# Kernel tuning notes

Measured on AMD Instinct MI355X. Metric: run time of the kernel, lower is better.

Reference implementation:

```python
import jax, jax.numpy as jnp
import numpy as np

RESOLUTION = 2048
NUM_BEAMS = 256
K0 = 50.0
TWO_PI = 2.0 * np.pi


def setup_inputs() -> dict:
    key = jax.random.key(0)
    ks = jax.random.split(key, 6)
    # meshgrid buffers (indexing='ij')
    x = jnp.linspace(-1.0, 1.0, RESOLUTION, dtype=jnp.float32)
    y = jnp.linspace(-1.0, 1.0, RESOLUTION, dtype=jnp.float32)
    X, Y = jnp.meshgrid(x, y, indexing='ij')
    return {
        'theta': jax.random.uniform(ks[0], (NUM_BEAMS,), jnp.float32) * TWO_PI,
        'real': jax.random.normal(ks[1], (NUM_BEAMS,), jnp.float32) * 0.1,
        'imag': jax.random.normal(ks[2], (NUM_BEAMS,), jnp.float32) * 0.1,
        'x0': jax.random.uniform(ks[3], (NUM_BEAMS,), jnp.float32) * 2.0 - 1.0,
        'y0': jax.random.uniform(ks[4], (NUM_BEAMS,), jnp.float32) * 2.0 - 1.0,
        'log_sigma': jnp.zeros((NUM_BEAMS,), jnp.float32),
        'X': X,
        'Y': Y,
    }


def reference(theta, real, imag, x0, y0, log_sigma, X, Y):
    # Accumulate E = sum_i coeff_i * exp(i*phase_i) * envelope_i over beams,
    # carrying (E_re, E_im) through a scan so only grid-sized buffers live at once.
    def body(carry, p):
        E_re, E_im = carry
        th, re, im, px, py, ls = p
        kx = K0 * jnp.cos(th)
        ky = K0 * jnp.sin(th)
        sigma = jnp.exp(ls) + 0.001
        env = jnp.exp(-((X - px) ** 2 + (Y - py) ** 2) / sigma ** 2)
        phase = kx * X + ky * Y
        c = jnp.cos(phase)
        s = jnp.sin(phase)
        # (re + i*im) * (c + i*s) * env
        E_re = E_re + env * (re * c - im * s)
        E_im = E_im + env * (re * s + im * c)
        return (E_re, E_im), None

    params = jnp.stack([theta, real, imag, x0, y0, log_sigma], axis=1)  # [B, 6]
    zero = jnp.zeros_like(X)
    (E_re, E_im), _ = jax.lax.scan(body, (zero, zero), params)
    return E_re ** 2 + E_im ** 2  # |E|^2
```

## Files before the change

kernel.cpp:

```cpp
#include <hip/hip_runtime.h>
#include <math.h>

#define RES 2048
#define NB  256
#define PLANE (RES * NB)
#define STEP (2.0f / 2047.0f)

typedef _Float16 f16;
typedef _Float16 f16x8 __attribute__((ext_vector_type(8)));
typedef float    f32x16 __attribute__((ext_vector_type(16)));

#define AS1 __attribute__((address_space(1)))
#define AS3 __attribute__((address_space(3)))

__device__ __forceinline__ void g2l16(const void* g, void* l) {
    __builtin_amdgcn_global_load_lds((const AS1 void*)g, (AS3 void*)l, 16, 0, 0);
}

__device__ __forceinline__ f16x8 neg8(f16x8 v) {
    union { f16x8 h; unsigned int u[4]; } x;
    x.h = v;
    #pragma unroll
    for (int i = 0; i < 4; ++i) x.u[i] ^= 0x80008000u;
    return x.h;
}


__global__ __launch_bounds__(256) void tables_frag(
    const float* __restrict__ theta, const float* __restrict__ reA,
    const float* __restrict__ imA, const float* __restrict__ x0A,
    const float* __restrict__ y0A, const float* __restrict__ lsA,
    f16* __restrict__ ws)
{
    __shared__ float4 sP0[NB];
    __shared__ float4 sP1[NB];

    const int t = threadIdx.x;
    {
        const int b = t;
        const float th = theta[b];
        const float s = __sinf(th), c = __cosf(th);
        const float sig = __expf(lsA[b]) + 0.001f;
        sP0[b] = make_float4(50.0f * c, 50.0f * s, x0A[b], y0A[b]);
        sP1[b] = make_float4(reA[b], imA[b], 1.0f / (sig * sig), 0.0f);
    }
    __syncthreads();

    f16* aRe = ws;
    f16* aIm = ws + PLANE;
    f16* bRe = ws + 2 * PLANE;
    f16* bIm = ws + 3 * PLANE;

    const int gid = blockIdx.x * 256 + t;
    const int l   = gid & 63;
    const int w   = gid >> 6;
    const int grow = (w >> 4) * 32 + (l & 31);
    const int b0   = (w & 15) * 16 + (l >> 5) * 8;
    const int e    = w * 512 + (l >> 5) * 256 + (l & 31) * 8;

    const float xv = -1.0f + (float)grow * STEP;

    float aRv[8], aIv[8], bRv[8], bIv[8];
    #pragma unroll
    for (int j = 0; j < 8; ++j) {
        const int b = b0 + j;
        const float4 p0 = sP0[b];
        const float4 p1 = sP1[b];

        const float phx = p0.x * xv;
        const float snx = __sinf(phx), csx = __cosf(phx);
        const float dx = xv - p0.z;
        const float ex = __expf(-dx * dx * p1.z);
        aRv[j] = ex * (p1.x * csx - p1.y * snx);
        aIv[j] = ex * (p1.x * snx + p1.y * csx);

        const float phy = p0.y * xv;
        const float sny = __sinf(phy), csy = __cosf(phy);
        const float dy = xv - p0.w;
        const float ey = __expf(-dy * dy * p1.z);
        bRv[j] = ey * csy;
        bIv[j] = ey * sny;
    }

    union { f16 h[8]; float4 v; } p;
    #pragma unroll
    for (int j = 0; j < 8; ++j) p.h[j] = (f16)aRv[j];
    *(float4*)&aRe[e] = p.v;
    #pragma unroll
    for (int j = 0; j < 8; ++j) p.h[j] = (f16)aIv[j];
    *(float4*)&aIm[e] = p.v;
    #pragma unroll
    for (int j = 0; j < 8; ++j) p.h[j] = (f16)bRv[j];
    *(float4*)&bRe[e] = p.v;
    #pragma unroll
    for (int j = 0; j < 8; ++j) p.h[j] = (f16)bIv[j];
    *(float4*)&bIm[e] = p.v;
}

__global__ __launch_bounds__(256) void gemm_lds(
    const f16* __restrict__ ws, float* __restrict__ out)
{
    __shared__ f16 lds[2][12 * 512];

    const int t    = threadIdx.x;
    const int lane = t & 63;
    const int wave = t >> 6;
    const int la   = lane & 31;
    const int lg   = lane >> 5;

    const int flat = blockIdx.x;
    const int swz  = (flat & 7) * 64 + (flat >> 3);
    const int mb   = swz >> 4;
    const int nb   = swz & 15;
    const int m0   = mb * 64;
    const int n0   = nb * 128;

    const f16* gsrc[3];
    int ldst[3];
    #pragma unroll
    for (int j = 0; j < 3; ++j) {
        const int idx = wave + 4 * j;
        int p, rb;
        if (idx < 2)      { p = 0; rb = (m0 >> 5) + idx; }
        else if (idx < 4) { p = 1; rb = (m0 >> 5) + (idx - 2); }
        else if (idx < 8) { p = 2; rb = (n0 >> 5) + (idx - 4); }
        else              { p = 3; rb = (n0 >> 5) + (idx - 8); }
        gsrc[j] = ws + (size_t)p * PLANE + rb * 16 * 512 + lane * 8;
        ldst[j] = idx * 512;
    }

    #define STAGE(bf, kt)                                                     \
    do {                                                                      \
        g2l16(gsrc[0] + (kt) * 512, &lds[bf][ldst[0]]);                       \
        g2l16(gsrc[1] + (kt) * 512, &lds[bf][ldst[1]]);                       \
        g2l16(gsrc[2] + (kt) * 512, &lds[bf][ldst[2]]);                       \
    } while (0)

    const int lo   = lane * 8;
    const int oAR0 = 0 * 512 + lo, oAR1 = 1 * 512 + lo;
    const int oAI0 = 2 * 512 + lo, oAI1 = 3 * 512 + lo;
    const int oBR  = (4 + wave) * 512 + lo;
    const int oBI  = (8 + wave) * 512 + lo;

    f32x16 accRe0 = (f32x16)0.0f, accIm0 = (f32x16)0.0f;
    f32x16 accRe1 = (f32x16)0.0f, accIm1 = (f32x16)0.0f;

    STAGE(0, 0);
    __syncthreads();

    for (int kt = 0; kt < 16; ++kt) {
        const int cur = kt & 1;
        if (kt + 1 < 16)
            STAGE(cur ^ 1, kt + 1);

        const f16* s = lds[cur];
        const f16x8 aR0 = *(const f16x8*)(s + oAR0);
        const f16x8 aR1 = *(const f16x8*)(s + oAR1);
        const f16x8 aI0 = *(const f16x8*)(s + oAI0);
        const f16x8 aI1 = *(const f16x8*)(s + oAI1);
        const f16x8 bR  = *(const f16x8*)(s + oBR);
        const f16x8 bI  = *(const f16x8*)(s + oBI);
        const f16x8 bN  = neg8(bI);

        __builtin_amdgcn_s_setprio(1);
        accRe0 = __builtin_amdgcn_mfma_f32_32x32x16_f16(aR0, bR, accRe0, 0, 0, 0);
        accIm0 = __builtin_amdgcn_mfma_f32_32x32x16_f16(aR0, bI, accIm0, 0, 0, 0);
        accRe1 = __builtin_amdgcn_mfma_f32_32x32x16_f16(aR1, bR, accRe1, 0, 0, 0);
        accIm1 = __builtin_amdgcn_mfma_f32_32x32x16_f16(aR1, bI, accIm1, 0, 0, 0);
        accRe0 = __builtin_amdgcn_mfma_f32_32x32x16_f16(aI0, bN, accRe0, 0, 0, 0);
        accIm0 = __builtin_amdgcn_mfma_f32_32x32x16_f16(aI0, bR, accIm0, 0, 0, 0);
        accRe1 = __builtin_amdgcn_mfma_f32_32x32x16_f16(aI1, bN, accRe1, 0, 0, 0);
        accIm1 = __builtin_amdgcn_mfma_f32_32x32x16_f16(aI1, bR, accIm1, 0, 0, 0);
        __builtin_amdgcn_s_setprio(0);

        __syncthreads();
    }

    const int gn = n0 + wave * 32 + la;
    #pragma unroll
    for (int r = 0; r < 16; ++r) {
        const int row = (r & 3) + 8 * (r >> 2) + 4 * lg;
        const float er = accRe0[r], ei = accIm0[r];
        out[(size_t)(m0 + row) * RES + gn] = er * er + ei * ei;
    }
    #pragma unroll
    for (int r = 0; r < 16; ++r) {
        const int row = (r & 3) + 8 * (r >> 2) + 4 * lg;
        const float er = accRe1[r], ei = accIm1[r];
        out[(size_t)(m0 + 32 + row) * RES + gn] = er * er + ei * ei;
    }
    #undef STAGE
}

__global__ __launch_bounds__(256) void ewald_direct(
    const float* __restrict__ theta, const float* __restrict__ reA,
    const float* __restrict__ imA, const float* __restrict__ x0A,
    const float* __restrict__ y0A, const float* __restrict__ lsA,
    const float* __restrict__ X, const float* __restrict__ Y,
    float* __restrict__ out)
{
    __shared__ float kxs[NB], kys[NB], res[NB], ims[NB], pxs[NB], pys[NB], is2s[NB];
    const int t = threadIdx.x;
    if (t < NB) {
        const float th  = theta[t];
        const float sig = __expf(lsA[t]) + 0.001f;
        kxs[t] = 50.0f * __cosf(th);
        kys[t] = 50.0f * __sinf(th);
        res[t] = reA[t]; ims[t] = imA[t];
        pxs[t] = x0A[t]; pys[t] = y0A[t];
        is2s[t] = 1.0f / (sig * sig);
    }
    __syncthreads();
    const size_t npix = (size_t)RES * RES;
    for (size_t idx = (size_t)blockIdx.x * blockDim.x + t; idx < npix;
         idx += (size_t)gridDim.x * blockDim.x) {
        const float xv = X[idx], yv = Y[idx];
        float er = 0.f, ei = 0.f;
        for (int b = 0; b < NB; ++b) {
            const float dx = xv - pxs[b], dy = yv - pys[b];
            const float env = __expf(-(dx * dx + dy * dy) * is2s[b]);
            const float ph = kxs[b] * xv + kys[b] * yv;
            float s, c;
            __sincosf(ph, &s, &c);
            er += env * (res[b] * c - ims[b] * s);
            ei += env * (res[b] * s + ims[b] * c);
        }
        out[idx] = er * er + ei * ei;
    }
}

extern "C" void kernel_launch(void* const* d_in, const int* in_sizes, int n_in,
                              void* d_out, int out_size, void* d_ws, size_t ws_size,
                              hipStream_t stream) {
    const float* theta = (const float*)d_in[0];
    const float* reA   = (const float*)d_in[1];
    const float* imA   = (const float*)d_in[2];
    const float* x0A   = (const float*)d_in[3];
    const float* y0A   = (const float*)d_in[4];
    const float* lsA   = (const float*)d_in[5];
    const float* X     = (const float*)d_in[6];
    const float* Y     = (const float*)d_in[7];
    float* out = (float*)d_out;

    const size_t need = 4 * (size_t)PLANE * sizeof(f16);

    if (ws_size >= need) {
        f16* ws = (f16*)d_ws;
        tables_frag<<<256, 256, 0, stream>>>(theta, reA, imA, x0A, y0A, lsA, ws);
        gemm_lds<<<512, 256, 0, stream>>>(ws, out);
    } else {
        ewald_direct<<<2048, 256, 0, stream>>>(theta, reA, imA, x0A, y0A, lsA,
                                               X, Y, out);
    }
}
```

Before: 22.07 us.

## Use 3-mult complex GEMM, triple-buffer LDS pipeline, split table kernel work

```diff
diff --git a/kernel.cpp b/kernel.cpp
--- a/kernel.cpp
+++ b/kernel.cpp
@@ -16,15 +16,6 @@
 __device__ __forceinline__ void g2l16(const void* g, void* l) {
     __builtin_amdgcn_global_load_lds((const AS1 void*)g, (AS3 void*)l, 16, 0, 0);
 }
-
-__device__ __forceinline__ f16x8 neg8(f16x8 v) {
-    union { f16x8 h; unsigned int u[4]; } x;
-    x.h = v;
-    #pragma unroll
-    for (int i = 0; i < 4; ++i) x.u[i] ^= 0x80008000u;
-    return x.h;
-}
-
 
 __global__ __launch_bounds__(256) void tables_frag(
     const float* __restrict__ theta, const float* __restrict__ reA,
@@ -51,18 +42,20 @@
     f16* bRe = ws + 2 * PLANE;
     f16* bIm = ws + 3 * PLANE;
 
-    const int gid = blockIdx.x * 256 + t;
-    const int l   = gid & 63;
-    const int w   = gid >> 6;
-    const int grow = (w >> 4) * 32 + (l & 31);
-    const int b0   = (w & 15) * 16 + (l >> 5) * 8;
-    const int e    = w * 512 + (l >> 5) * 256 + (l & 31) * 8;
+    const int gid   = blockIdx.x * 256 + t;
+    const int l     = gid & 63;
+    const int w2    = gid >> 6;
+    const int chunk = w2 >> 1;
+    const int half  = w2 & 1;
+    const int grow  = (chunk >> 4) * 32 + (l & 31);
+    const int b0    = (chunk & 15) * 16 + (l >> 5) * 8 + half * 4;
+    const int e     = chunk * 512 + (l >> 5) * 256 + (l & 31) * 8 + half * 4;
 
     const float xv = -1.0f + (float)grow * STEP;
 
-    float aRv[8], aIv[8], bRv[8], bIv[8];
-    #pragma unroll
-    for (int j = 0; j < 8; ++j) {
+    float aRv[4], aIv[4], bRv[4], bIv[4];
+    #pragma unroll
+    for (int j = 0; j < 4; ++j) {
         const int b = b0 + j;
         const float4 p0 = sP0[b];
         const float4 p1 = sP1[b];
@@ -82,25 +75,25 @@
         bIv[j] = ey * sny;
     }
 
-    union { f16 h[8]; float4 v; } p;
-    #pragma unroll
-    for (int j = 0; j < 8; ++j) p.h[j] = (f16)aRv[j];
-    *(float4*)&aRe[e] = p.v;
-    #pragma unroll
-    for (int j = 0; j < 8; ++j) p.h[j] = (f16)aIv[j];
-    *(float4*)&aIm[e] = p.v;
-    #pragma unroll
-    for (int j = 0; j < 8; ++j) p.h[j] = (f16)bRv[j];
-    *(float4*)&bRe[e] = p.v;
-    #pragma unroll
-    for (int j = 0; j < 8; ++j) p.h[j] = (f16)bIv[j];
-    *(float4*)&bIm[e] = p.v;
+    union { f16 h[4]; float2 v; } p;
+    #pragma unroll
+    for (int j = 0; j < 4; ++j) p.h[j] = (f16)aRv[j];
+    *(float2*)&aRe[e] = p.v;
+    #pragma unroll
+    for (int j = 0; j < 4; ++j) p.h[j] = (f16)aIv[j];
+    *(float2*)&aIm[e] = p.v;
+    #pragma unroll
+    for (int j = 0; j < 4; ++j) p.h[j] = (f16)bRv[j];
+    *(float2*)&bRe[e] = p.v;
+    #pragma unroll
+    for (int j = 0; j < 4; ++j) p.h[j] = (f16)bIv[j];
+    *(float2*)&bIm[e] = p.v;
 }
 
 __global__ __launch_bounds__(256) void gemm_lds(
     const f16* __restrict__ ws, float* __restrict__ out)
 {
-    __shared__ f16 lds[2][12 * 512];
+    __shared__ f16 lds[3][12 * 512];
 
     const int t    = threadIdx.x;
     const int lane = t & 63;
@@ -110,10 +103,8 @@
 
     const int flat = blockIdx.x;
     const int swz  = (flat & 7) * 64 + (flat >> 3);
-    const int mb   = swz >> 4;
-    const int nb   = swz & 15;
-    const int m0   = mb * 64;
-    const int n0   = nb * 128;
+    const int m0   = (swz >> 4) * 64;
+    const int n0   = (swz & 15) * 128;
 
     const f16* gsrc[3];
     int ldst[3];
@@ -131,9 +122,9 @@
 
     #define STAGE(bf, kt)                                                     \
     do {                                                                      \
-        g2l16(gsrc[0] + (kt) * 512, &lds[bf][ldst[0]]);                       \
-        g2l16(gsrc[1] + (kt) * 512, &lds[bf][ldst[1]]);                       \
-        g2l16(gsrc[2] + (kt) * 512, &lds[bf][ldst[2]]);                       \
+        g2l16(gsrc[0] + (kt) * 512, &lds[0][0] + (bf) * 6144 + ldst[0]);      \
+        g2l16(gsrc[1] + (kt) * 512, &lds[0][0] + (bf) * 6144 + ldst[1]);      \
+        g2l16(gsrc[2] + (kt) * 512, &lds[0][0] + (bf) * 6144 + ldst[2]);      \
     } while (0)
 
     const int lo   = lane * 8;
@@ -142,51 +133,56 @@
     const int oBR  = (4 + wave) * 512 + lo;
     const int oBI  = (8 + wave) * 512 + lo;
 
-    f32x16 accRe0 = (f32x16)0.0f, accIm0 = (f32x16)0.0f;
-    f32x16 accRe1 = (f32x16)0.0f, accIm1 = (f32x16)0.0f;
+    f32x16 t1_0 = (f32x16)0.0f, t2_0 = (f32x16)0.0f, t3_0 = (f32x16)0.0f;
+    f32x16 t1_1 = (f32x16)0.0f, t2_1 = (f32x16)0.0f, t3_1 = (f32x16)0.0f;
 
     STAGE(0, 0);
-    __syncthreads();
-
+    STAGE(1, 1);
+
+    int cur = 0;
     for (int kt = 0; kt < 16; ++kt) {
-        const int cur = kt & 1;
-        if (kt + 1 < 16)
-            STAGE(cur ^ 1, kt + 1);
-
-        const f16* s = lds[cur];
+        asm volatile("s_waitcnt vmcnt(3)" ::: "memory");
+        __builtin_amdgcn_s_barrier();
+
+        int nx = cur - 1; if (nx < 0) nx += 3;
+        STAGE(nx, (kt + 2) & 15);
+
+        const f16* s = &lds[0][0] + cur * 6144;
         const f16x8 aR0 = *(const f16x8*)(s + oAR0);
         const f16x8 aR1 = *(const f16x8*)(s + oAR1);
         const f16x8 aI0 = *(const f16x8*)(s + oAI0);
         const f16x8 aI1 = *(const f16x8*)(s + oAI1);
         const f16x8 bR  = *(const f16x8*)(s + oBR);
         const f16x8 bI  = *(const f16x8*)(s + oBI);
-        const f16x8 bN  = neg8(bI);
+        const f16x8 aS0 = aR0 + aI0;
+        const f16x8 aS1 = aR1 + aI1;
+        const f16x8 bS  = bR + bI;
 
         __builtin_amdgcn_s_setprio(1);
-        accRe0 = __builtin_amdgcn_mfma_f32_32x32x16_f16(aR0, bR, accRe0, 0, 0, 0);
-        accIm0 = __builtin_amdgcn_mfma_f32_32x32x16_f16(aR0, bI, accIm0, 0, 0, 0);
-        accRe1 = __builtin_amdgcn_mfma_f32_32x32x16_f16(aR1, bR, accRe1, 0, 0, 0);
-        accIm1 = __builtin_amdgcn_mfma_f32_32x32x16_f16(aR1, bI, accIm1, 0, 0, 0);
-        accRe0 = __builtin_amdgcn_mfma_f32_32x32x16_f16(aI0, bN, accRe0, 0, 0, 0);
-        accIm0 = __builtin_amdgcn_mfma_f32_32x32x16_f16(aI0, bR, accIm0, 0, 0, 0);
-        accRe1 = __builtin_amdgcn_mfma_f32_32x32x16_f16(aI1, bN, accRe1, 0, 0, 0);
-        accIm1 = __builtin_amdgcn_mfma_f32_32x32x16_f16(aI1, bR, accIm1, 0, 0, 0);
+        t1_0 = __builtin_amdgcn_mfma_f32_32x32x16_f16(aR0, bR, t1_0, 0, 0, 0);
+        t2_0 = __builtin_amdgcn_mfma_f32_32x32x16_f16(aI0, bI, t2_0, 0, 0, 0);
+        t3_0 = __builtin_amdgcn_mfma_f32_32x32x16_f16(aS0, bS, t3_0, 0, 0, 0);
+        t1_1 = __builtin_amdgcn_mfma_f32_32x32x16_f16(aR1, bR, t1_1, 0, 0, 0);
+        t2_1 = __builtin_amdgcn_mfma_f32_32x32x16_f16(aI1, bI, t2_1, 0, 0, 0);
+        t3_1 = __builtin_amdgcn_mfma_f32_32x32x16_f16(aS1, bS, t3_1, 0, 0, 0);
         __builtin_amdgcn_s_setprio(0);
 
-        __syncthreads();
+        cur = cur + 1 == 3 ? 0 : cur + 1;
     }
 
     const int gn = n0 + wave * 32 + la;
     #pragma unroll
     for (int r = 0; r < 16; ++r) {
         const int row = (r & 3) + 8 * (r >> 2) + 4 * lg;
-        const float er = accRe0[r], ei = accIm0[r];
+        const float er = t1_0[r] - t2_0[r];
+        const float ei = t3_0[r] - t1_0[r] - t2_0[r];
         out[(size_t)(m0 + row) * RES + gn] = er * er + ei * ei;
     }
     #pragma unroll
     for (int r = 0; r < 16; ++r) {
         const int row = (r & 3) + 8 * (r >> 2) + 4 * lg;
-        const float er = accRe1[r], ei = accIm1[r];
+        const float er = t1_1[r] - t2_1[r];
+        const float ei = t3_1[r] - t1_1[r] - t2_1[r];
         out[(size_t)(m0 + 32 + row) * RES + gn] = er * er + ei * ei;
     }
     #undef STAGE
@@ -246,7 +242,7 @@
 
     if (ws_size >= need) {
         f16* ws = (f16*)d_ws;
-        tables_frag<<<256, 256, 0, stream>>>(theta, reA, imA, x0A, y0A, lsA, ws);
+        tables_frag<<<512, 256, 0, stream>>>(theta, reA, imA, x0A, y0A, lsA, ws);
         gemm_lds<<<512, 256, 0, stream>>>(ws, out);
     } else {
         ewald_direct<<<2048, 256, 0, stream>>>(theta, reA, imA, x0A, y0A, lsA,
```

Measured after the change: 22.92 us. +3.9%, slower.
